# Optimization experiments

Measured on AMD Instinct MI355X. Metric: run time of the kernel, lower is better.

Reference implementation:

```python
import math
import jax, jax.numpy as jnp
import numpy as np

# --- Cayley-Dickson octonion structure constants: e_i * e_j = sign * e_{i XOR j} ---
def _cd_tables(levels=3):
    idx = np.array([[0]]); sgn = np.array([[1]])
    for _ in range(levels):
        n = idx.shape[0]; N = 2 * n
        I = np.zeros((N, N), np.int64); S = np.zeros((N, N), np.int64)
        cj = lambda j: 1 if j == 0 else -1  # conj sign of basis element j
        for i in range(n):
            for j in range(n):
                I[i, j] = idx[i, j];             S[i, j] = sgn[i, j]
                I[i, n + j] = n + idx[j, i];     S[i, n + j] = sgn[j, i]
                I[n + i, j] = n + idx[i, j];     S[n + i, j] = sgn[i, j] * cj(j)
                I[n + i, n + j] = idx[j, i];     S[n + i, n + j] = -cj(j) * sgn[j, i]
        idx, sgn = I, S
    return idx, sgn

_OIDX, _OSGN = _cd_tables()
# Octonion-structured linear: out_i = sum_j SIGN[i,j] * x_j @ W[WIDX[i,j]], WIDX[i,j]=i^j
_WIDX = np.array([[i ^ j for j in range(8)] for i in range(8)], np.int64)
_SIGN = np.array([[_OSGN[j, i ^ j] for j in range(8)] for i in range(8)], np.float32)


def _oct_linear(x, W):
    # x: [B,T,C], W: [8, C/8, C/8]
    B, T, C = x.shape
    Cp = C // 8
    parts = x.reshape(B, T, 8, Cp)
    Weff = jnp.asarray(_SIGN)[:, :, None, None] * W[jnp.asarray(_WIDX)]  # [8,8,Cp,Cp]
    return jnp.einsum('btjp,ijpq->btiq', parts, Weff).reshape(B, T, C)


def _rope(x, cos, sin):
    # x: [B,T,H,D]; consecutive channel pairs form complex numbers
    B, T, H, D = x.shape
    xr = x.reshape(B, T, H, D // 2, 2)
    xe, xo = xr[..., 0], xr[..., 1]
    c = cos[None, :, None, :]
    s = sin[None, :, None, :]
    return jnp.stack([xe * c - xo * s, xe * s + xo * c], axis=-1).reshape(B, T, H, D)


def _forward(x, Wq, Wk, Wv, Wo, mixer_W, mixer_beta, freqs_cos, freqs_sin):
    B, T, C = x.shape
    H = 32; D = C // H
    q = _oct_linear(x, Wq).reshape(B, T, H, D)
    k = _oct_linear(x, Wk).reshape(B, T, H, D)
    v = _oct_linear(x, Wv).reshape(B, T, H, D)
    q = _rope(q, freqs_cos, freqs_sin)
    k = _rope(k, freqs_cos, freqs_sin)
    q = q.transpose(0, 2, 1, 3)  # [B,H,T,D]
    k = k.transpose(0, 2, 1, 3)
    v = v.transpose(0, 2, 1, 3)
    scores = jnp.einsum('bhqd,bhkd->bhqk', q, k) / jnp.sqrt(jnp.float32(D))
    mask = jnp.tril(jnp.ones((T, T), bool))
    scores = jnp.where(mask, scores, jnp.finfo(scores.dtype).min)
    y = jnp.einsum('bhqk,bhkd->bhqd', jax.nn.softmax(scores, axis=-1), v)  # [B,H,T,D]
    # octonion head mixing in groups of 8 heads
    G = H // 8
    yg = y.reshape(B, G, 8, T, D)
    Weff = jnp.asarray(_SIGN)[:, :, None, None] * mixer_W[jnp.asarray(_WIDX)]  # [8,8,D,D]
    mixed = jnp.einsum('bgjtd,ijde->bgite', yg, Weff) * mixer_beta
    y = mixed.reshape(B, H, T, D).transpose(0, 2, 1, 3).reshape(B, T, C)
    return _oct_linear(y, Wo)


def setup_inputs() -> dict:
    key = jax.random.key(0)
    ks = jax.random.split(key, 8)
    B, T, C, H = 1, 2048, 4096, 32
    D = C // H; Cp = C // 8
    x = jax.random.normal(ks[0], (B, T, C), jnp.float32)
    Wq = jax.random.normal(ks[1], (8, Cp, Cp), jnp.float32) * 0.02
    Wk = jax.random.normal(ks[2], (8, Cp, Cp), jnp.float32) * 0.02
    Wv = jax.random.normal(ks[3], (8, Cp, Cp), jnp.float32) * 0.02
    Wo = jax.random.normal(ks[4], (8, Cp, Cp), jnp.float32) * 0.02
    mixer_W = jax.random.normal(ks[5], (8, D, D), jnp.float32) * 0.02
    mixer_beta = jnp.ones((D,), jnp.float32) * np.float32(math.sqrt(3.0 / (2.0 * D)))
    half = D // 2
    inv = 1.0 / (10000.0 ** (np.arange(half) * 2.0 / D))
    ang = np.arange(T)[:, None] * inv[None, :]
    freqs_cos = jnp.asarray(np.cos(ang), jnp.float32)
    freqs_sin = jnp.asarray(np.sin(ang), jnp.float32)
    return dict(x=x, Wq=Wq, Wk=Wk, Wv=Wv, Wo=Wo, mixer_W=mixer_W,
                mixer_beta=mixer_beta, freqs_cos=freqs_cos, freqs_sin=freqs_sin)


def reference(x, Wq, Wk, Wv, Wo, mixer_W, mixer_beta, freqs_cos, freqs_sin):
    return _forward(x, Wq, Wk, Wv, Wo, mixer_W, mixer_beta, freqs_cos, freqs_sin)
```

## Files before the change

kernel.cpp:

```cpp
#include <hip/hip_runtime.h>

typedef float f32x4 __attribute__((ext_vector_type(4)));
typedef __bf16 bf16x8 __attribute__((ext_vector_type(8)));
typedef unsigned short u16;
typedef u16 u16x8 __attribute__((ext_vector_type(8)));

__constant__ float c_osgn[64] = {
  1, 1, 1, 1, 1, 1, 1, 1,
  1,-1, 1,-1, 1,-1,-1, 1,
  1,-1,-1, 1, 1, 1,-1,-1,
  1, 1,-1,-1, 1,-1, 1,-1,
  1,-1,-1,-1,-1, 1, 1, 1,
  1, 1,-1, 1,-1,-1,-1, 1,
  1, 1, 1,-1,-1, 1,-1,-1,
  1,-1, 1, 1,-1,-1, 1,-1
};

__device__ __forceinline__ u16 f2bf(float f) {
  union { float f; unsigned u; } v; v.f = f;
  unsigned u = v.u;
  return (u16)((u + 0x7fffu + ((u >> 16) & 1u)) >> 16);
}
__device__ __forceinline__ float bf2f(u16 h) {
  union { unsigned u; float f; } v; v.u = ((unsigned)h) << 16;
  return v.f;
}

typedef const __attribute__((address_space(1))) void* as1cv;
typedef __attribute__((address_space(3))) void* as3v;
__device__ __forceinline__ void load16_lds(const void* g, void* l) {
  __builtin_amdgcn_global_load_lds((as1cv)g, (as3v)l, 16, 0, 0);
}

__global__ void conv_f32_bf16_vec(const float* __restrict__ src, u16* __restrict__ dst) {
  int i = blockIdx.x * 256 + threadIdx.x;
  float4 v = ((const float4*)src)[i];
  ushort4 o; o.x = f2bf(v.x); o.y = f2bf(v.y); o.z = f2bf(v.z); o.w = f2bf(v.w);
  ((ushort4*)dst)[i] = o;
}

__global__ __launch_bounds__(256) void transpose_w4(
    const float* __restrict__ Wq, const float* __restrict__ Wk,
    const float* __restrict__ Wv, const float* __restrict__ Wo,
    u16* __restrict__ WtB, long wsz) {
  __shared__ float t[64][65];
  const int zw = blockIdx.z;
  const int wsel = zw >> 3, w = zw & 7;
  const float* W = (wsel == 0) ? Wq : (wsel == 1) ? Wk : (wsel == 2) ? Wv : Wo;
  u16* Wt = WtB + wsel * wsz;
  const int p0 = blockIdx.y * 64, q0 = blockIdx.x * 64;
  const float* src = W + ((long)w * 512 + p0) * 512 + q0;
  const int tid = threadIdx.x;
  const int r = tid >> 2, c0 = (tid & 3) * 16;
#pragma unroll
  for (int j = 0; j < 4; j++) {
    float4 v = *(const float4*)(src + (long)r * 512 + c0 + j * 4);
    t[r][c0 + j * 4 + 0] = v.x; t[r][c0 + j * 4 + 1] = v.y;
    t[r][c0 + j * 4 + 2] = v.z; t[r][c0 + j * 4 + 3] = v.w;
  }
  __syncthreads();
  u16* dst = Wt + ((long)w * 512 + q0) * 512 + p0;
#pragma unroll
  for (int j = 0; j < 2; j++) {
    u16x8 o;
#pragma unroll
    for (int k = 0; k < 8; k++) o[k] = f2bf(t[c0 + j * 8 + k][r]);
    *(u16x8*)(dst + (long)r * 512 + c0 + j * 8) = o;
  }
}

__global__ void transpose_wm(const float* __restrict__ W, const float* __restrict__ beta,
                             u16* __restrict__ Wt) {
  int idx = blockIdx.x * 256 + threadIdx.x;
  int w = idx >> 14, rem = idx & 16383;
  int e = rem >> 7, d = rem & 127;
  Wt[(w << 14) + (e << 7) + d] = f2bf(W[(w << 14) + (d << 7) + e] * beta[e]);
}

template <int MODE>
__global__ __launch_bounds__(256, 3) void oct_gemm128(
    const u16* __restrict__ A, const u16* __restrict__ WtB,
    void* __restrict__ out0, void* __restrict__ out1, void* __restrict__ out2,
    const float* __restrict__ fc, const float* __restrict__ fs,
    int K, int lda, int ldo,
    int slab_shift, int bs_shift, long wslab, long oslab, long acolslab)
{
  __shared__ u16 smem[16384];
  const int NT = K >> 6;
  const int BS = 1 << bs_shift;
  const long wblk = (long)BS * BS;

  const int nwg = gridDim.x * gridDim.y;
  const int lin = blockIdx.y * gridDim.x + blockIdx.x;
  const int swz = (lin & 7) * (nwg >> 3) + (lin >> 3);
  const int bx = swz % gridDim.x, by = swz / gridDim.x;

  const int nglob = bx * 128;
  const int z = nglob >> slab_shift;
  const int np = nglob & ((1 << slab_shift) - 1);
  const int bi = np >> bs_shift;
  const int nsub = np & (BS - 1);
  const int bm = by * 128;
  const u16* Wt = WtB + (long)z * wslab;
  const long acol0 = (long)z * acolslab;

  const int tid = threadIdx.x;
  const int lane = tid & 63, w = tid >> 6;
  const int l15 = lane & 15, lg = lane >> 4;
  const int wm = w >> 1, wn = w & 1;
  const int srow = lane >> 3;
  const int sgr  = (lane & 7) ^ srow;

  f32x4 acc[4][4];
#pragma unroll
  for (int a = 0; a < 4; a++)
#pragma unroll
    for (int b = 0; b < 4; b++) acc[a][b] = f32x4{0.f, 0.f, 0.f, 0.f};

  for (int t = 0; t < NT; ++t) {
    const int k0 = t << 6;
    const int bj = k0 >> bs_shift;
    const int widx = bi ^ bj;
    const unsigned xm = (c_osgn[bj * 8 + widx] < 0.f) ? 0x80008000u : 0u;
    const u16* Wsrc = Wt + (long)widx * wblk + (k0 & (BS - 1));

#pragma unroll
    for (int i = 0; i < 4; i++) {
      const int r = (w * 4 + i) * 8;
      load16_lds(A + (long)(bm + r + srow) * lda + acol0 + k0 + sgr * 8,
                 (void*)(smem + r * 64));
    }
#pragma unroll
    for (int i = 0; i < 4; i++) {
      const int r = (w * 4 + i) * 8;
      load16_lds(Wsrc + (long)(nsub + r + srow) * BS + sgr * 8,
                 (void*)(smem + 8192 + r * 64));
    }
    __syncthreads();

#pragma unroll
    for (int kk = 0; kk < 64; kk += 32) {
      const int gsw = (((kk >> 3) + lg) ^ (l15 & 7)) * 8;
      uint4 a4[4];
      bf16x8 bF[4];
#pragma unroll
      for (int mt = 0; mt < 4; mt++)
        a4[mt] = *(const uint4*)(smem + (wm * 64 + mt * 16 + l15) * 64 + gsw);
      if (xm) {
#pragma unroll
        for (int mt = 0; mt < 4; mt++) {
          a4[mt].x ^= xm; a4[mt].y ^= xm; a4[mt].z ^= xm; a4[mt].w ^= xm;
        }
      }
#pragma unroll
      for (int nt = 0; nt < 4; nt++)
        bF[nt] = *(const bf16x8*)(smem + 8192 + (wn * 64 + nt * 16 + l15) * 64 + gsw);
#pragma unroll
      for (int mt = 0; mt < 4; mt++)
#pragma unroll
        for (int nt = 0; nt < 4; nt++)
          acc[mt][nt] = __builtin_amdgcn_mfma_f32_16x16x32_bf16(
              *(const bf16x8*)&a4[mt], bF[nt], acc[mt][nt], 0, 0, 0);
    }
    __syncthreads();
  }

  if constexpr (MODE == 1) {
    if (z == 2) {
      u16* vT = (u16*)out2;
      const int h = np >> 7;
#pragma unroll
      for (int dh = 0; dh < 2; ++dh) {
        if (wn == dh) {
#pragma unroll
          for (int mt = 0; mt < 4; mt++)
#pragma unroll
            for (int nt = 0; nt < 4; nt++)
#pragma unroll
              for (int j = 0; j < 4; j++)
                smem[(nt * 16 + l15) * 144 + wm * 64 + mt * 16 + 4 * lg + j] =
                    f2bf(acc[mt][nt][j]);
        }
        __syncthreads();
#pragma unroll
        for (int p = 0; p < 4; ++p) {
          const int dl = p * 16 + (tid >> 4);
          const int tt = (tid & 15) * 8;
          u16x8 o = *(const u16x8*)(smem + dl * 144 + tt);
          *(u16x8*)(vT + ((long)h * 128 + dh * 64 + dl) * 2048 + bm + tt) = o;
        }
        __syncthreads();
      }
    } else {
      u16* dq = (u16*)(z == 0 ? out0 : out1);
      const int h = np >> 7;
#pragma unroll
      for (int mt = 0; mt < 4; mt++)
#pragma unroll
        for (int nt = 0; nt < 4; nt++) {
          const int d = wn * 64 + nt * 16 + l15;
          const int p = d >> 1;
          const bool ev = (l15 & 1) == 0;
#pragma unroll
          for (int j = 0; j < 4; j++) {
            const int trow = bm + wm * 64 + mt * 16 + 4 * lg + j;
            const float v = acc[mt][nt][j];
            const float sh = __shfl_xor(v, 1);
            const float c = fc[trow * 64 + p];
            const float s = fs[trow * 64 + p];
            const float o = ev ? (v * c - sh * s) : (sh * s + v * c);
            dq[((long)h * 2048 + trow) * 128 + d] = f2bf(o);
          }
        }
    }
  } else {
#pragma unroll
    for (int mt = 0; mt < 4; mt++)
#pragma unroll
      for (int nt = 0; nt < 4; nt++)
#pragma unroll
        for (int j = 0; j < 4; j++) {
          const int row = bm + wm * 64 + mt * 16 + 4 * lg + j;
          const int col = np + wn * 64 + nt * 16 + l15;
          const float v = acc[mt][nt][j];
          if constexpr (MODE == 0)
            ((u16*)out0)[(long)z * oslab + (long)row * ldo + col] = f2bf(v);
          else
            ((float*)out0)[(long)row * ldo + col] = v;
        }
  }
}

__global__ __launch_bounds__(256, 2) void attn4(
    const u16* __restrict__ qR, const u16* __restrict__ kR,
    const u16* __restrict__ vT, u16* __restrict__ y)
{
  const int bid = blockIdx.x;
  const int h = bid & 31;
  const int qb = 31 - (bid >> 5);
  const int q0 = qb * 64;

  const int tid = threadIdx.x;
  const int lane = tid & 63, w = tid >> 6;
  const int l15 = lane & 15, lg = lane >> 4;

  __shared__ u16 Ks[2][64][128];
  __shared__ u16 Vs[2][128][64];
  __shared__ u16 Ps[4][16][64];

  auto stageK = [&](int kb, int buf) {
    const long kbase = (long)h * 2048 + (long)kb * 64;
#pragma unroll
    for (int i = 0; i < 4; i++) {
      const int j = w * 4 + i;
      const int row = j * 4 + (lane >> 4);
      const int sg = (lane & 15) ^ (row & 7);
      load16_lds(kR + (kbase + row) * 128 + sg * 8, (void*)&Ks[buf][j * 4][0]);
    }
  };
  auto stageV = [&](int kb, int buf) {
    const long vbase = (long)h * 128 * 2048 + (long)kb * 64;
#pragma unroll
    for (int i = 0; i < 4; i++) {
      const int j = w * 4 + i;
      const int row = j * 8 + (lane >> 3);
      const int sg = (lane & 7) ^ (row & 7);
      load16_lds(vT + vbase + (long)row * 2048 + sg * 8, (void*)&Vs[buf][j * 8][0]);
    }
  };

  stageK(0, 0);
  stageV(0, 0);

  bf16x8 aQ[4];
  {
    const long qbase = ((long)h * 2048 + q0 + w * 16 + l15) * 128;
#pragma unroll
    for (int c = 0; c < 4; c++)
      aQ[c] = *(const bf16x8*)(qR + qbase + 32 * c + 8 * lg);
  }

  float m[4], lsum[4];
  f32x4 Y[8];
#pragma unroll
  for (int rr = 0; rr < 4; rr++) { m[rr] = -1e30f; lsum[rr] = 0.f; }
#pragma unroll
  for (int dt = 0; dt < 8; dt++) Y[dt] = f32x4{0.f, 0.f, 0.f, 0.f};

  const float scale = 0.08838834764831845f;
  const int nkb = qb + 1;

  for (int kb = 0; kb < nkb; kb++) {
    const int buf = kb & 1;
    const int k0 = kb * 64;
    if (kb + 1 < nkb) { stageK(kb + 1, buf ^ 1); stageV(kb + 1, buf ^ 1); }
    if (kb + 1 < nkb) asm volatile("s_waitcnt vmcnt(8)" ::: "memory");
    else              asm volatile("s_waitcnt vmcnt(0)" ::: "memory");
    __builtin_amdgcn_s_barrier();
    asm volatile("" ::: "memory");

    f32x4 S[4];
#pragma unroll
    for (int ks = 0; ks < 4; ks++) S[ks] = f32x4{0.f, 0.f, 0.f, 0.f};
#pragma unroll
    for (int c = 0; c < 4; c++) {
      bf16x8 bK[4];
#pragma unroll
      for (int ks = 0; ks < 4; ks++)
        bK[ks] = *(const bf16x8*)&Ks[buf][ks * 16 + l15][(((4 * c + lg) ^ (l15 & 7)) * 8)];
#pragma unroll
      for (int ks = 0; ks < 4; ks++)
        S[ks] = __builtin_amdgcn_mfma_f32_16x16x32_bf16(aQ[c], bK[ks], S[ks], 0, 0, 0);
    }

    {
      const int qrow0 = q0 + w * 16 + 4 * lg;
#pragma unroll
      for (int ks = 0; ks < 4; ks++) {
        const int kg = k0 + ks * 16 + l15;
#pragma unroll
        for (int rr = 0; rr < 4; rr++) {
          float s = S[ks][rr] * scale;
          S[ks][rr] = (kg > qrow0 + rr) ? -1e30f : s;
        }
      }
      float sf[4];
      bool need = false;
#pragma unroll
      for (int rr = 0; rr < 4; rr++) {
        float mx = fmaxf(fmaxf(S[0][rr], S[1][rr]), fmaxf(S[2][rr], S[3][rr]));
#pragma unroll
        for (int off = 1; off < 16; off <<= 1) mx = fmaxf(mx, __shfl_xor(mx, off));
        const bool upd = (mx > m[rr] + 8.f);
        const float mn = upd ? mx : m[rr];
        const float sc = upd ? __expf(m[rr] - mn) : 1.f;
        need |= upd;
        m[rr] = mn;
        float rsum = 0.f;
#pragma unroll
        for (int ks = 0; ks < 4; ks++) {
          float e = __expf(S[ks][rr] - mn);
          S[ks][rr] = e;
          rsum += e;
        }
#pragma unroll
        for (int off = 1; off < 16; off <<= 1) rsum += __shfl_xor(rsum, off);
        lsum[rr] = lsum[rr] * sc + rsum;
        sf[rr] = sc;
      }
      if (__any(need)) {
#pragma unroll
        for (int dt = 0; dt < 8; dt++) {
          f32x4 yv = Y[dt];
          yv[0] *= sf[0]; yv[1] *= sf[1]; yv[2] *= sf[2]; yv[3] *= sf[3];
          Y[dt] = yv;
        }
      }
#pragma unroll
      for (int ks = 0; ks < 4; ks++)
#pragma unroll
        for (int rr = 0; rr < 4; rr++) {
          const int row = 4 * lg + rr;
          const int G = (2 * ks + (l15 >> 3)) ^ (row & 7);
          Ps[w][row][G * 8 + (l15 & 7)] = f2bf(S[ks][rr]);
        }
    }

#pragma unroll
    for (int kk = 0; kk < 2; kk++) {
      const int pg = ((4 * kk + lg) ^ (l15 & 7)) * 8;
      bf16x8 pF = *(const bf16x8*)&Ps[w][l15][pg];
#pragma unroll
      for (int dt = 0; dt < 8; dt++) {
        bf16x8 vF = *(const bf16x8*)&Vs[buf][dt * 16 + l15][pg];
        Y[dt] = __builtin_amdgcn_mfma_f32_16x16x32_bf16(pF, vF, Y[dt], 0, 0, 0);
      }
    }
    asm volatile("" ::: "memory");
    __builtin_amdgcn_s_barrier();
    asm volatile("" ::: "memory");
  }

  float inv[4];
#pragma unroll
  for (int rr = 0; rr < 4; rr++) inv[rr] = 1.0f / lsum[rr];
#pragma unroll
  for (int dt = 0; dt < 8; dt++)
#pragma unroll
    for (int rr = 0; rr < 4; rr++)
      y[(long)(q0 + w * 16 + 4 * lg + rr) * 4096 + h * 128 + dt * 16 + l15] =
          f2bf(Y[dt][rr] * inv[rr]);
}

extern "C" void kernel_launch(void* const* d_in, const int* in_sizes, int n_in,
                              void* d_out, int out_size, void* d_ws, size_t ws_size,
                              hipStream_t stream) {
  const float* x    = (const float*)d_in[0];
  const float* Wq   = (const float*)d_in[1];
  const float* Wk   = (const float*)d_in[2];
  const float* Wv   = (const float*)d_in[3];
  const float* Wo   = (const float*)d_in[4];
  const float* Wm   = (const float*)d_in[5];
  const float* beta = (const float*)d_in[6];
  const float* fc   = (const float*)d_in[7];
  const float* fs   = (const float*)d_in[8];
  float* out = (float*)d_out;

  const long TC = 2048L * 4096L;
  const long WSZ = 8L * 512 * 512;
  u16* ws  = (u16*)d_ws;
  u16* xb  = ws;
  u16* wt  = ws + TC;
  u16* wmt = wt + 4 * WSZ;
  u16* g3  = wmt + 131072L;
  u16* r3  = g3 + 3 * TC;
  u16* yatt = xb;
  u16* ymix = g3;

  conv_f32_bf16_vec<<<TC / 4 / 256, 256, 0, stream>>>(x, xb);
  transpose_w4<<<dim3(8, 8, 32), 256, 0, stream>>>(Wq, Wk, Wv, Wo, wt, WSZ);
  transpose_wm<<<512, 256, 0, stream>>>(Wm, beta, wmt);

  oct_gemm128<1><<<dim3(96, 16), 256, 0, stream>>>(
      xb, wt, (void*)r3, (void*)(r3 + TC), (void*)(r3 + 2 * TC), fc, fs,
      4096, 4096, 4096, 12, 9, WSZ, 0L, 0L);

  attn4<<<1024, 256, 0, stream>>>(r3, r3 + TC, r3 + 2 * TC, yatt);

  oct_gemm128<0><<<dim3(32, 16), 256, 0, stream>>>(
      yatt, wmt, (void*)ymix, nullptr, nullptr, nullptr, nullptr,
      1024, 4096, 4096, 10, 7, 0L, 1024L, 1024L);

  oct_gemm128<2><<<dim3(32, 16), 256, 0, stream>>>(
      ymix, wt + 3 * WSZ, (void*)out, nullptr, nullptr, nullptr, nullptr,
      4096, 4096, 4096, 12, 9, 0L, 0L, 0L);
}
```

Baseline: 439.6 us.

## Fuse Q/K/V octonion GEMMs into one kernel sharing the A tile

```diff
diff --git a/kernel.cpp b/kernel.cpp
--- a/kernel.cpp
+++ b/kernel.cpp
@@ -77,11 +77,146 @@
   Wt[(w << 14) + (e << 7) + d] = f2bf(W[(w << 14) + (d << 7) + e] * beta[e]);
 }
 
+__global__ __launch_bounds__(256, 2) void oct_gemmQKV(
+    const u16* __restrict__ A, const u16* __restrict__ WtB,
+    u16* __restrict__ out0, u16* __restrict__ out1, u16* __restrict__ out2,
+    const float* __restrict__ fc, const float* __restrict__ fs, long wsz)
+{
+  __shared__ u16 smem[32768];
+
+  const int nwg = gridDim.x * gridDim.y;
+  const int lin = blockIdx.y * gridDim.x + blockIdx.x;
+  const int swz = (lin & 7) * (nwg >> 3) + (lin >> 3);
+  const int bx = swz % gridDim.x, by = swz / gridDim.x;
+
+  const int np = bx * 128;
+  const int bi = np >> 9;
+  const int nsub = np & 511;
+  const int bm = by * 128;
+  const int h = np >> 7;
+
+  const int tid = threadIdx.x;
+  const int lane = tid & 63, w = tid >> 6;
+  const int l15 = lane & 15, lg = lane >> 4;
+  const int wm = w >> 1, wn = w & 1;
+  const int srow = lane >> 3;
+  const int sgr  = (lane & 7) ^ srow;
+
+  f32x4 acc[3][4][4];
+#pragma unroll
+  for (int z = 0; z < 3; z++)
+#pragma unroll
+    for (int a = 0; a < 4; a++)
+#pragma unroll
+      for (int b = 0; b < 4; b++) acc[z][a][b] = f32x4{0.f, 0.f, 0.f, 0.f};
+
+  for (int t = 0; t < 64; ++t) {
+    const int k0 = t << 6;
+    const int bj = t >> 3;
+    const int widx = bi ^ bj;
+    const unsigned xm = (c_osgn[bj * 8 + widx] < 0.f) ? 0x80008000u : 0u;
+    const long woff = (long)widx * 262144 + (k0 & 511);
+
+#pragma unroll
+    for (int i = 0; i < 4; i++) {
+      const int r = (w * 4 + i) * 8;
+      load16_lds(A + (long)(bm + r + srow) * 4096 + k0 + sgr * 8,
+                 (void*)(smem + r * 64));
+    }
+#pragma unroll
+    for (int z = 0; z < 3; z++) {
+      const u16* Wsrc = WtB + (long)z * wsz + woff;
+#pragma unroll
+      for (int i = 0; i < 4; i++) {
+        const int r = (w * 4 + i) * 8;
+        load16_lds(Wsrc + (long)(nsub + r + srow) * 512 + sgr * 8,
+                   (void*)(smem + 8192 * (1 + z) + r * 64));
+      }
+    }
+    __syncthreads();
+
+#pragma unroll
+    for (int kk = 0; kk < 64; kk += 32) {
+      const int gsw = (((kk >> 3) + lg) ^ (l15 & 7)) * 8;
+      uint4 a4[4];
+#pragma unroll
+      for (int mt = 0; mt < 4; mt++)
+        a4[mt] = *(const uint4*)(smem + (wm * 64 + mt * 16 + l15) * 64 + gsw);
+      if (xm) {
+#pragma unroll
+        for (int mt = 0; mt < 4; mt++) {
+          a4[mt].x ^= xm; a4[mt].y ^= xm; a4[mt].z ^= xm; a4[mt].w ^= xm;
+        }
+      }
+#pragma unroll
+      for (int z = 0; z < 3; z++) {
+        bf16x8 bF[4];
+#pragma unroll
+        for (int nt = 0; nt < 4; nt++)
+          bF[nt] = *(const bf16x8*)(smem + 8192 * (1 + z) +
+                                    (wn * 64 + nt * 16 + l15) * 64 + gsw);
+#pragma unroll
+        for (int mt = 0; mt < 4; mt++)
+#pragma unroll
+          for (int nt = 0; nt < 4; nt++)
+            acc[z][mt][nt] = __builtin_amdgcn_mfma_f32_16x16x32_bf16(
+                *(const bf16x8*)&a4[mt], bF[nt], acc[z][mt][nt], 0, 0, 0);
+      }
+    }
+    __syncthreads();
+  }
+
+#pragma unroll
+  for (int z = 0; z < 2; z++) {
+    u16* dq = (z == 0) ? out0 : out1;
+#pragma unroll
+    for (int mt = 0; mt < 4; mt++)
+#pragma unroll
+      for (int nt = 0; nt < 4; nt++) {
+        const int d = wn * 64 + nt * 16 + l15;
+        const int p = d >> 1;
+        const bool ev = (l15 & 1) == 0;
+#pragma unroll
+        for (int j = 0; j < 4; j++) {
+          const int trow = bm + wm * 64 + mt * 16 + 4 * lg + j;
+          const float v = acc[z][mt][nt][j];
+          const float sh = __shfl_xor(v, 1);
+          const float c = fc[trow * 64 + p];
+          const float s = fs[trow * 64 + p];
+          const float o = ev ? (v * c - sh * s) : (sh * s + v * c);
+          dq[((long)h * 2048 + trow) * 128 + d] = f2bf(o);
+        }
+      }
+  }
+
+#pragma unroll
+  for (int dh = 0; dh < 2; ++dh) {
+    __syncthreads();
+    if (wn == dh) {
+#pragma unroll
+      for (int mt = 0; mt < 4; mt++)
+#pragma unroll
+        for (int nt = 0; nt < 4; nt++)
+#pragma unroll
+          for (int j = 0; j < 4; j++)
+            smem[(nt * 16 + l15) * 152 + wm * 64 + mt * 16 + 4 * lg + j] =
+                f2bf(acc[2][mt][nt][j]);
+    }
+    __syncthreads();
+#pragma unroll
+    for (int p = 0; p < 4; ++p) {
+      const int dl = p * 16 + (tid >> 4);
+      const int tt = (tid & 15) * 8;
+      u16x8 o = *(const u16x8*)(smem + dl * 152 + tt);
+      *(u16x8*)(out2 + ((long)h * 128 + dh * 64 + dl) * 2048 + bm + tt) = o;
+    }
+  }
+}
+
 template <int MODE>
 __global__ __launch_bounds__(256, 3) void oct_gemm128(
     const u16* __restrict__ A, const u16* __restrict__ WtB,
-    void* __restrict__ out0, void* __restrict__ out1, void* __restrict__ out2,
-    const float* __restrict__ fc, const float* __restrict__ fs,
+    void* __restrict__ out0,
     int K, int lda, int ldo,
     int slab_shift, int bs_shift, long wslab, long oslab, long acolslab)
 {
@@ -165,70 +300,20 @@
     __syncthreads();
   }
 
-  if constexpr (MODE == 1) {
-    if (z == 2) {
-      u16* vT = (u16*)out2;
-      const int h = np >> 7;
-#pragma unroll
-      for (int dh = 0; dh < 2; ++dh) {
-        if (wn == dh) {
-#pragma unroll
-          for (int mt = 0; mt < 4; mt++)
-#pragma unroll
-            for (int nt = 0; nt < 4; nt++)
-#pragma unroll
-              for (int j = 0; j < 4; j++)
-                smem[(nt * 16 + l15) * 144 + wm * 64 + mt * 16 + 4 * lg + j] =
-                    f2bf(acc[mt][nt][j]);
-        }
-        __syncthreads();
-#pragma unroll
-        for (int p = 0; p < 4; ++p) {
-          const int dl = p * 16 + (tid >> 4);
-          const int tt = (tid & 15) * 8;
-          u16x8 o = *(const u16x8*)(smem + dl * 144 + tt);
-          *(u16x8*)(vT + ((long)h * 128 + dh * 64 + dl) * 2048 + bm + tt) = o;
-        }
-        __syncthreads();
-      }
-    } else {
-      u16* dq = (u16*)(z == 0 ? out0 : out1);
-      const int h = np >> 7;
-#pragma unroll
-      for (int mt = 0; mt < 4; mt++)
-#pragma unroll
-        for (int nt = 0; nt < 4; nt++) {
-          const int d = wn * 64 + nt * 16 + l15;
-          const int p = d >> 1;
-          const bool ev = (l15 & 1) == 0;
-#pragma unroll
-          for (int j = 0; j < 4; j++) {
-            const int trow = bm + wm * 64 + mt * 16 + 4 * lg + j;
-            const float v = acc[mt][nt][j];
-            const float sh = __shfl_xor(v, 1);
-            const float c = fc[trow * 64 + p];
-            const float s = fs[trow * 64 + p];
-            const float o = ev ? (v * c - sh * s) : (sh * s + v * c);
-            dq[((long)h * 2048 + trow) * 128 + d] = f2bf(o);
-          }
-        }
-    }
-  } else {
-#pragma unroll
-    for (int mt = 0; mt < 4; mt++)
-#pragma unroll
-      for (int nt = 0; nt < 4; nt++)
-#pragma unroll
-        for (int j = 0; j < 4; j++) {
-          const int row = bm + wm * 64 + mt * 16 + 4 * lg + j;
-          const int col = np + wn * 64 + nt * 16 + l15;
-          const float v = acc[mt][nt][j];
-          if constexpr (MODE == 0)
-            ((u16*)out0)[(long)z * oslab + (long)row * ldo + col] = f2bf(v);
-          else
-            ((float*)out0)[(long)row * ldo + col] = v;
-        }
-  }
+#pragma unroll
+  for (int mt = 0; mt < 4; mt++)
+#pragma unroll
+    for (int nt = 0; nt < 4; nt++)
+#pragma unroll
+      for (int j = 0; j < 4; j++) {
+        const int row = bm + wm * 64 + mt * 16 + 4 * lg + j;
+        const int col = np + wn * 64 + nt * 16 + l15;
+        const float v = acc[mt][nt][j];
+        if constexpr (MODE == 0)
+          ((u16*)out0)[(long)z * oslab + (long)row * ldo + col] = f2bf(v);
+        else
+          ((float*)out0)[(long)row * ldo + col] = v;
+      }
 }
 
 __global__ __launch_bounds__(256, 2) void attn4(
@@ -421,17 +506,16 @@
   transpose_w4<<<dim3(8, 8, 32), 256, 0, stream>>>(Wq, Wk, Wv, Wo, wt, WSZ);
   transpose_wm<<<512, 256, 0, stream>>>(Wm, beta, wmt);
 
-  oct_gemm128<1><<<dim3(96, 16), 256, 0, stream>>>(
-      xb, wt, (void*)r3, (void*)(r3 + TC), (void*)(r3 + 2 * TC), fc, fs,
-      4096, 4096, 4096, 12, 9, WSZ, 0L, 0L);
+  oct_gemmQKV<<<dim3(32, 16), 256, 0, stream>>>(
+      xb, wt, r3, r3 + TC, r3 + 2 * TC, fc, fs, WSZ);
 
   attn4<<<1024, 256, 0, stream>>>(r3, r3 + TC, r3 + 2 * TC, yatt);
 
   oct_gemm128<0><<<dim3(32, 16), 256, 0, stream>>>(
-      yatt, wmt, (void*)ymix, nullptr, nullptr, nullptr, nullptr,
+      yatt, wmt, (void*)ymix,
       1024, 4096, 4096, 10, 7, 0L, 1024L, 1024L);
 
   oct_gemm128<2><<<dim3(32, 16), 256, 0, stream>>>(
-      ymix, wt + 3 * WSZ, (void*)out, nullptr, nullptr, nullptr, nullptr,
+      ymix, wt + 3 * WSZ, (void*)out,
       4096, 4096, 4096, 12, 9, 0L, 0L, 0L);
 }
```

After: 422.9 us. 3.8% less time.
